# Optimization experiments

Measured on AMD Instinct MI355X. Metric: run time of the kernel, lower is better.

## Reference

```python
import jax, jax.numpy as jnp
import numpy as np

N_NODES = 50000
N_EDGES = 800000
F_IN = 128
HEADS = 4
C_OUT = 32
NEG_SLOPE = 0.2
BN_EPS = 1e-5


def _add_self_loops(edge_index, edge_attr, n):
    # PyG fill_value='mean': self-loop attr = mean of incoming edge attrs per node (0 if none)
    src, dst = edge_index[0], edge_index[1]
    deg = jax.ops.segment_sum(jnp.ones_like(edge_attr[:, 0]), dst, num_segments=n)
    loop_attr = jax.ops.segment_sum(edge_attr, dst, num_segments=n) / jnp.maximum(deg, 1.0)[:, None]
    loop = jnp.arange(n)
    src2 = jnp.concatenate([src, loop])
    dst2 = jnp.concatenate([dst, loop])
    attr2 = jnp.concatenate([edge_attr, loop_attr], axis=0)
    return src2, dst2, attr2


def _segment_softmax(logits, seg, n):
    m = jax.ops.segment_max(logits, seg, num_segments=n)
    m = jnp.where(jnp.isfinite(m), m, 0.0)
    ex = jnp.exp(logits - m[seg])
    s = jax.ops.segment_sum(ex, seg, num_segments=n)
    return ex / s[seg]


def _gatv2(x, src, dst, eattr, Wl, bl, Wr, br, We, att, bias, n):
    # x: [n, F]; returns [n, HEADS*C_OUT]
    xl = (x @ Wl + bl).reshape(n, HEADS, C_OUT)
    xr = (x @ Wr + br).reshape(n, HEADS, C_OUT)
    ea = (eattr @ We).reshape(-1, HEADS, C_OUT)
    xlj = xl[src]                                   # [E, H, C] gather
    msg = jax.nn.leaky_relu(xlj + xr[dst] + ea, NEG_SLOPE)
    logits = jnp.einsum('ehc,hc->eh', msg, att)     # [E, H]
    alpha = _segment_softmax(logits, dst, n)
    out = jax.ops.segment_sum(xlj * alpha[..., None], dst, num_segments=n)
    return out.reshape(n, HEADS * C_OUT) + bias


def _batchnorm(x, gamma, beta):
    mu = x.mean(axis=0)
    var = x.var(axis=0)
    return gamma * (x - mu) * jax.lax.rsqrt(var + BN_EPS) + beta


def setup_inputs() -> dict:
    key = jax.random.key(0)
    ks = jax.random.split(key, 20)
    HC = HEADS * C_OUT
    s = 0.05
    inp = {
        'emb': jax.random.normal(ks[0], (N_NODES, F_IN), dtype=jnp.float32),
        'edge_index': jax.random.randint(ks[1], (2, N_EDGES), 0, N_NODES, dtype=jnp.int64),
        'edge_weight': jax.random.uniform(ks[2], (N_EDGES, 1), dtype=jnp.float32),
        'Wl1': jax.random.normal(ks[3], (F_IN, HC)) * s,
        'bl1': jnp.zeros((HC,), jnp.float32),
        'Wr1': jax.random.normal(ks[4], (F_IN, HC)) * s,
        'br1': jnp.zeros((HC,), jnp.float32),
        'We1': jax.random.normal(ks[5], (1, HC)) * s,
        'att1': jax.random.normal(ks[6], (HEADS, C_OUT)) * s,
        'bias1': jnp.zeros((HC,), jnp.float32),
        'gamma1': jnp.ones((HC,), jnp.float32),
        'beta1': jnp.zeros((HC,), jnp.float32),
        'Wl2': jax.random.normal(ks[7], (HC, HC)) * s,
        'bl2': jnp.zeros((HC,), jnp.float32),
        'Wr2': jax.random.normal(ks[8], (HC, HC)) * s,
        'br2': jnp.zeros((HC,), jnp.float32),
        'We2': jax.random.normal(ks[9], (1, HC)) * s,
        'att2': jax.random.normal(ks[10], (HEADS, C_OUT)) * s,
        'bias2': jnp.zeros((HC,), jnp.float32),
    }
    return inp


def reference(emb, edge_index, edge_weight, Wl1, bl1, Wr1, br1, We1, att1, bias1,
              gamma1, beta1, Wl2, bl2, Wr2, br2, We2, att2, bias2):
    n = emb.shape[0]
    src, dst, eattr = _add_self_loops(edge_index, edge_weight, n)
    h1 = _gatv2(emb, src, dst, eattr, Wl1, bl1, Wr1, br1, We1, att1, bias1, n)
    h1 = jax.nn.elu(_batchnorm(h1, gamma1, beta1))
    h2 = _gatv2(h1, src, dst, eattr, Wl2, bl2, Wr2, br2, We2, att2, bias2, n)
    # fusion: mean over [input_emb, h1, h2] along stacked axis
    return (emb + h1 + h2) / 3.0
```

## Files before the change

kernel.cpp:

```cpp
#include <hip/hip_runtime.h>
#include <hip/hip_bf16.h>
#include <math.h>

#define N_NODES 50000
#define N_EDGES 800000
#define HC 128
#define SLOT 64

#define BM 128
#define NBX ((N_NODES + BM - 1) / BM)
#define NCHK 64
#define EPB (N_EDGES / NCHK)
#define NRNG 4
#define RNG_N (N_NODES / NRNG)
#define RNG_W (RNG_N / 2)
#define NW (N_NODES / 2)
#define NSCAT (NCHK * NRNG)
#define NB2 ((NW + 255) / 256)

typedef short bh8 __attribute__((ext_vector_type(8)));
typedef float f4 __attribute__((ext_vector_type(4)));
typedef float f2 __attribute__((ext_vector_type(2)));

__device__ __forceinline__ unsigned int pk2(float a, float b) {
  return (unsigned int)__bfloat16_as_ushort(__float2bfloat16(a)) |
         ((unsigned int)__bfloat16_as_ushort(__float2bfloat16(b)) << 16);
}
__device__ __forceinline__ float blo(unsigned int u) { return __uint_as_float(u << 16); }
__device__ __forceinline__ float bhi(unsigned int u) { return __uint_as_float(u & 0xffff0000u); }
__device__ __forceinline__ f2 vmax2(f2 a, f2 b) {
#if __has_builtin(__builtin_elementwise_max)
  return __builtin_elementwise_max(a, b);
#else
  f2 r; r.x = fmaxf(a.x, b.x); r.y = fmaxf(a.y, b.y); return r;
#endif
}

__global__ __launch_bounds__(256) void k_histprep(
    const float* __restrict__ Wl1, const float* __restrict__ Wr1,
    const float* __restrict__ Wl2, const float* __restrict__ Wr2,
    unsigned short* __restrict__ WtAll,
    float* __restrict__ chsum, float* __restrict__ chsq,
    const int* __restrict__ ei, unsigned int* __restrict__ counts32) {
  __shared__ unsigned int hist[RNG_W];
  int tid = threadIdx.x, bid = blockIdx.x;
  int gid = bid * 256 + tid;
  {
    int m = gid >> 14;
    int idx = gid & 16383;
    const float* src = (m == 0) ? Wl1 : (m == 1) ? Wr1 : (m == 2) ? Wl2 : Wr2;
    int k = idx >> 7, n = idx & 127;
    WtAll[((size_t)m * HC + n) * HC + k] =
        __bfloat16_as_ushort(__float2bfloat16(src[k * HC + n]));
    if (gid < HC) { chsum[gid] = 0.f; chsq[gid] = 0.f; }
  }
  int c = bid >> 2, r = bid & 3;
  int rb = r * RNG_N;
  for (int w = tid; w < RNG_W; w += 256) hist[w] = 0u;
  __syncthreads();
  const int* dstp = ei + N_EDGES + c * EPB;
  for (int g = tid; g < EPB / 4; g += 256) {
    int4 d4 = *(const int4*)(dstp + g * 4);
    int dl;
    dl = d4.x - rb; if ((unsigned)dl < RNG_N) atomicAdd(&hist[dl >> 1], (dl & 1) ? 0x10000u : 1u);
    dl = d4.y - rb; if ((unsigned)dl < RNG_N) atomicAdd(&hist[dl >> 1], (dl & 1) ? 0x10000u : 1u);
    dl = d4.z - rb; if ((unsigned)dl < RNG_N) atomicAdd(&hist[dl >> 1], (dl & 1) ? 0x10000u : 1u);
    dl = d4.w - rb; if ((unsigned)dl < RNG_N) atomicAdd(&hist[dl >> 1], (dl & 1) ? 0x10000u : 1u);
  }
  __syncthreads();
  unsigned int* dst = counts32 + (size_t)c * NW + r * RNG_W;
  for (int w = tid; w < RNG_W; w += 256) dst[w] = hist[w];
}

__global__ __launch_bounds__(256) void k_scan(const unsigned int* __restrict__ counts32,
                                              unsigned int* __restrict__ bases32,
                                              int* __restrict__ cursor,
                                              int* __restrict__ counts2) {
  __shared__ int dh[80];
  int tid = threadIdx.x;
  int w = blockIdx.x * 256 + tid;
  if (tid < 80) dh[tid] = 0;
  __syncthreads();
  if (w < NW) {
    unsigned int a0 = 0, a1 = 0;
#pragma unroll 4
    for (int b = 0; b < NCHK; ++b) {
      unsigned int v = counts32[(size_t)b * NW + w];
      bases32[(size_t)b * NW + w] = a0 | (a1 << 16);
      a0 += v & 0xffffu;
      a1 += v >> 16;
    }
    cursor[2 * w] = (int)a0;
    cursor[2 * w + 1] = (int)a1;
    atomicAdd(&dh[min((int)a0, SLOT)], 1);
    atomicAdd(&dh[min((int)a1, SLOT)], 1);
  }
  __syncthreads();
  if (tid <= SLOT) counts2[blockIdx.x * 72 + tid] = dh[tid];
}

__global__ __launch_bounds__(256) void k_dprefix(const int* __restrict__ counts2,
                                                 int* __restrict__ bases2) {
  __shared__ int colsum[80], cbase[80];
  int d = threadIdx.x;
  if (d <= SLOT) {
    int s = 0;
    for (int b = 0; b < NB2; ++b) s += counts2[b * 72 + d];
    colsum[d] = s;
  }
  __syncthreads();
  if (d == 0) {
    int a = 0;
    for (int i = 0; i <= SLOT; ++i) { cbase[i] = a; a += colsum[i]; }
  }
  __syncthreads();
  if (d <= SLOT) {
    int a = cbase[d];
    for (int b = 0; b < NB2; ++b) { bases2[b * 72 + d] = a; a += counts2[b * 72 + d]; }
  }
}

__global__ __launch_bounds__(256) void k_scat_g1(
    const int* __restrict__ ei, const float* __restrict__ ew,
    const unsigned int* __restrict__ bases32, unsigned int* __restrict__ slots,
    const float* __restrict__ X, const unsigned short* __restrict__ Wt,
    const float* __restrict__ b0, const float* __restrict__ b1,
    unsigned short* __restrict__ Y0b, float* __restrict__ Y1,
    const int* __restrict__ cursor, const int* __restrict__ bases2,
    int* __restrict__ perm) {
  __shared__ __align__(16) unsigned int lsbuf[16384];
  int tid = threadIdx.x, bid = blockIdx.x;
  if (bid >= NSCAT + NBX) {
    int b2 = bid - NSCAT - NBX;
    int* dcur = (int*)lsbuf;
    if (tid <= SLOT) dcur[tid] = bases2[b2 * 72 + tid];
    __syncthreads();
    for (int i = tid; i < 512; i += 256) {
      int nn = b2 * 512 + i;
      if (nn < N_NODES) {
        int d = min(cursor[nn], SLOT);
        int pos = atomicAdd(&dcur[d], 1);
        perm[pos] = nn;
      }
    }
    return;
  }
  if (bid < NSCAT) {
    int c = bid >> 2, r = bid & 3;
    int rb = r * RNG_N;
    const unsigned int* bp = bases32 + (size_t)c * NW + r * RNG_W;
    for (int w = tid; w < RNG_W; w += 256) lsbuf[w] = bp[w];
    __syncthreads();
    const int* sp = ei + c * EPB;
    const int* dp = ei + N_EDGES + c * EPB;
    const float* wp = ew + c * EPB;
    for (int g = tid; g < EPB / 4; g += 256) {
      int4 s4 = *(const int4*)(sp + g * 4);
      int4 d4 = *(const int4*)(dp + g * 4);
      float4 w4 = *(const float4*)(wp + g * 4);
      int ss[4] = {s4.x, s4.y, s4.z, s4.w};
      int dd[4] = {d4.x, d4.y, d4.z, d4.w};
      float ww[4] = {w4.x, w4.y, w4.z, w4.w};
#pragma unroll
      for (int i = 0; i < 4; ++i) {
        int dl = dd[i] - rb;
        if ((unsigned)dl < RNG_N) {
          unsigned int old = atomicAdd(&lsbuf[dl >> 1], (dl & 1) ? 0x10000u : 1u);
          unsigned int pos = (dl & 1) ? (old >> 16) : (old & 0xffffu);
          unsigned int wq = min((unsigned int)(ww[i] * 65536.f + 0.5f), 65535u);
          if (pos < SLOT)
            slots[(size_t)dd[i] * SLOT + pos] = ((unsigned int)ss[i] << 16) | wq;
        }
      }
    }
    return;
  }
  unsigned short* Xls = (unsigned short*)lsbuf;
  unsigned short* Wls = Xls + 128 * 128;
  int row0 = (bid - NSCAT) * BM;
  {
    int r = tid >> 1;
    int ks = (tid & 1) * 64;
    int gr = row0 + r;
    const float* xp = X + (size_t)gr * HC + ks;
    int sw = r & 15;
#pragma unroll
    for (int i = 0; i < 4; ++i) {
      float f[16];
      if (gr < N_NODES) {
        *(float4*)&f[0] = *(const float4*)(xp + i * 16);
        *(float4*)&f[4] = *(const float4*)(xp + i * 16 + 4);
        *(float4*)&f[8] = *(const float4*)(xp + i * 16 + 8);
        *(float4*)&f[12] = *(const float4*)(xp + i * 16 + 12);
      } else {
#pragma unroll
        for (int j = 0; j < 16; ++j) f[j] = 0.f;
      }
      int kg = (ks >> 3) + i * 2;
      *(uint4*)&Xls[r * 128 + ((kg ^ sw) * 8)] =
          make_uint4(pk2(f[0], f[1]), pk2(f[2], f[3]), pk2(f[4], f[5]), pk2(f[6], f[7]));
      *(uint4*)&Xls[r * 128 + (((kg + 1) ^ sw) * 8)] =
          make_uint4(pk2(f[8], f[9]), pk2(f[10], f[11]), pk2(f[12], f[13]), pk2(f[14], f[15]));
    }
  }
  int lane = tid & 63;
  int wv = tid >> 6;
  int lrow = lane & 15;
  int lq = lane >> 4;
  int rbase = wv * 32;
#pragma unroll
  for (int half = 0; half < 2; ++half) {
    if (half) __syncthreads();
    {
      int n = tid >> 1;
      int ks2 = (tid & 1) * 64;
      const unsigned short* wp = Wt + half * (HC * HC) + n * HC + ks2;
      int swn = n & 15;
#pragma unroll
      for (int g = 0; g < 8; ++g) {
        uint4 v = *(const uint4*)(wp + g * 8);
        int kg = (ks2 >> 3) + g;
        *(uint4*)&Wls[n * 128 + ((kg ^ swn) * 8)] = v;
      }
    }
    __syncthreads();
    f4 acc[2][8];
#pragma unroll
    for (int mt = 0; mt < 2; ++mt)
#pragma unroll
      for (int nt = 0; nt < 8; ++nt) acc[mt][nt] = (f4){0.f, 0.f, 0.f, 0.f};
#pragma unroll
    for (int kk = 0; kk < 4; ++kk) {
      int kg = kk * 4 + lq;
      bh8 a0 = *(const bh8*)&Xls[(rbase + lrow) * 128 + ((kg ^ lrow) * 8)];
      bh8 a1 = *(const bh8*)&Xls[(rbase + 16 + lrow) * 128 + ((kg ^ lrow) * 8)];
#pragma unroll
      for (int nt = 0; nt < 8; ++nt) {
        bh8 b = *(const bh8*)&Wls[(nt * 16 + lrow) * 128 + ((kg ^ lrow) * 8)];
        acc[0][nt] = __builtin_amdgcn_mfma_f32_16x16x32_bf16(a0, b, acc[0][nt], 0, 0, 0);
        acc[1][nt] = __builtin_amdgcn_mfma_f32_16x16x32_bf16(a1, b, acc[1][nt], 0, 0, 0);
      }
    }
    const float* bb = half ? b1 : b0;
    float bv[8];
#pragma unroll
    for (int nt = 0; nt < 8; ++nt) bv[nt] = bb[nt * 16 + lrow];
#pragma unroll
    for (int mt = 0; mt < 2; ++mt) {
#pragma unroll
      for (int rr = 0; rr < 4; ++rr) {
        int gr = row0 + rbase + mt * 16 + lq * 4 + rr;
        if (gr < N_NODES) {
          if (half == 0) {
#pragma unroll
            for (int nt = 0; nt < 8; ++nt)
              Y0b[(size_t)gr * HC + nt * 16 + lrow] =
                  __bfloat16_as_ushort(__float2bfloat16(acc[mt][nt][rr] + bv[nt]));
          } else {
#pragma unroll
            for (int nt = 0; nt < 8; ++nt)
              Y1[(size_t)gr * HC + nt * 16 + lrow] = acc[mt][nt][rr] + bv[nt];
          }
        }
      }
    }
  }
}

__global__ __launch_bounds__(256) void k_gemm2(
    const unsigned short* __restrict__ Xb, const unsigned short* __restrict__ Wt,
    const float* __restrict__ b0, const float* __restrict__ b1,
    unsigned char* __restrict__ Y0f8, float* __restrict__ Y1,
    const float* __restrict__ chsum, const float* __restrict__ chsq,
    const float* __restrict__ gamma, const float* __restrict__ beta) {
  __shared__ __align__(16) unsigned short Xls[128 * 128];
  __shared__ __align__(16) unsigned short Wls[128 * 128];
  __shared__ float ssc[HC], ssh[HC];
  int tid = threadIdx.x;
  if (tid < HC) {
    float mu = chsum[tid] * (1.f / N_NODES);
    float var = chsq[tid] * (1.f / N_NODES) - mu * mu;
    float sc = gamma[tid] * rsqrtf(var + 1e-5f);
    ssc[tid] = sc;
    ssh[tid] = beta[tid] - mu * sc;
  }
  __syncthreads();
  int row0 = blockIdx.x * BM;
  {
    int r = tid >> 1;
    int ks = (tid & 1) * 64;
    int gr = row0 + r;
    const unsigned short* xp = Xb + (size_t)gr * HC + ks;
    int sw = r & 15;
#pragma unroll
    for (int i = 0; i < 4; ++i) {
      float f[16];
      if (gr < N_NODES) {
        uint4 ua = *(const uint4*)(xp + i * 16);
        uint4 ub = *(const uint4*)(xp + i * 16 + 8);
        f[0] = blo(ua.x); f[1] = bhi(ua.x); f[2] = blo(ua.y); f[3] = bhi(ua.y);
        f[4] = blo(ua.z); f[5] = bhi(ua.z); f[6] = blo(ua.w); f[7] = bhi(ua.w);
        f[8] = blo(ub.x); f[9] = bhi(ub.x); f[10] = blo(ub.y); f[11] = bhi(ub.y);
        f[12] = blo(ub.z); f[13] = bhi(ub.z); f[14] = blo(ub.w); f[15] = bhi(ub.w);
      } else {
#pragma unroll
        for (int j = 0; j < 16; ++j) f[j] = 0.f;
      }
#pragma unroll
      for (int j = 0; j < 16; ++j) {
        float y = fmaf(f[j], ssc[ks + i * 16 + j], ssh[ks + i * 16 + j]);
        f[j] = (y > 0.f) ? y : (__expf(y) - 1.f);
      }
      int kg = (ks >> 3) + i * 2;
      *(uint4*)&Xls[r * 128 + ((kg ^ sw) * 8)] =
          make_uint4(pk2(f[0], f[1]), pk2(f[2], f[3]), pk2(f[4], f[5]), pk2(f[6], f[7]));
      *(uint4*)&Xls[r * 128 + (((kg + 1) ^ sw) * 8)] =
          make_uint4(pk2(f[8], f[9]), pk2(f[10], f[11]), pk2(f[12], f[13]), pk2(f[14], f[15]));
    }
  }
  int lane = tid & 63;
  int wv = tid >> 6;
  int lrow = lane & 15;
  int lq = lane >> 4;
  int rbase = wv * 32;
#pragma unroll
  for (int half = 0; half < 2; ++half) {
    if (half) __syncthreads();
    {
      int n = tid >> 1;
      int ks = (tid & 1) * 64;
      const unsigned short* wp = Wt + half * (HC * HC) + n * HC + ks;
      int swn = n & 15;
#pragma unroll
      for (int g = 0; g < 8; ++g) {
        uint4 v = *(const uint4*)(wp + g * 8);
        int kg = (ks >> 3) + g;
        *(uint4*)&Wls[n * 128 + ((kg ^ swn) * 8)] = v;
      }
    }
    __syncthreads();
    f4 acc[2][8];
#pragma unroll
    for (int mt = 0; mt < 2; ++mt)
#pragma unroll
      for (int nt = 0; nt < 8; ++nt) acc[mt][nt] = (f4){0.f, 0.f, 0.f, 0.f};
#pragma unroll
    for (int kk = 0; kk < 4; ++kk) {
      int kg = kk * 4 + lq;
      bh8 a0 = *(const bh8*)&Xls[(rbase + lrow) * 128 + ((kg ^ lrow) * 8)];
      bh8 a1 = *(const bh8*)&Xls[(rbase + 16 + lrow) * 128 + ((kg ^ lrow) * 8)];
#pragma unroll
      for (int nt = 0; nt < 8; ++nt) {
        bh8 b = *(const bh8*)&Wls[(nt * 16 + lrow) * 128 + ((kg ^ lrow) * 8)];
        acc[0][nt] = __builtin_amdgcn_mfma_f32_16x16x32_bf16(a0, b, acc[0][nt], 0, 0, 0);
        acc[1][nt] = __builtin_amdgcn_mfma_f32_16x16x32_bf16(a1, b, acc[1][nt], 0, 0, 0);
      }
    }
    const float* bb = half ? b1 : b0;
    float bv[8];
#pragma unroll
    for (int nt = 0; nt < 8; ++nt) bv[nt] = bb[nt * 16 + lrow];
#pragma unroll
    for (int mt = 0; mt < 2; ++mt) {
#pragma unroll
      for (int rr = 0; rr < 4; ++rr) {
        int gr = row0 + rbase + mt * 16 + lq * 4 + rr;
        if (gr < N_NODES) {
          if (half == 0) {
#pragma unroll
            for (int nt = 0; nt < 8; ++nt) {
              float v = acc[mt][nt][rr] + bv[nt];
              int p = __builtin_amdgcn_cvt_pk_fp8_f32(v, v, 0, false);
              Y0f8[(size_t)gr * HC + nt * 16 + lrow] = (unsigned char)(p & 0xff);
            }
          } else {
#pragma unroll
            for (int nt = 0; nt < 8; ++nt)
              Y1[(size_t)gr * HC + nt * 16 + lrow] = acc[mt][nt][rr] + bv[nt];
          }
        }
      }
    }
  }
}

template <int FINAL, int F8>
__global__ __launch_bounds__(256) void k_gat(
    const void* __restrict__ xlv, const float* __restrict__ xr,
    const int* __restrict__ cursor, const unsigned int* __restrict__ slots,
    const int* __restrict__ perm,
    const float* __restrict__ We, const float* __restrict__ att,
    const float* __restrict__ bias, void* __restrict__ out,
    const float* __restrict__ emb, const unsigned short* __restrict__ h1p,
    const float* __restrict__ chsum, const float* __restrict__ chsq,
    const float* __restrict__ gamma, const float* __restrict__ beta) {
  int g = threadIdx.x >> 5;
  int lane = threadIdx.x & 31;
  int n = perm[blockIdx.x * 8 + g];
  int fi = n * 32 + lane;
  const uint2* xl2 = (const uint2*)xlv;
  const unsigned int* xf = (const unsigned int*)xlv;
  float4 xr4 = ((const float4*)xr)[fi];
  float4 we4 = ((const float4*)We)[lane];
  float4 at4 = ((const float4*)att)[lane];
  const float LOG2E = 1.4426950408889634f;
  const float WSC = 1.f / 65536.f;
  f2 xr01 = {xr4.x, xr4.y}, xr23 = {xr4.z, xr4.w};
  f2 we01 = {we4.x * WSC, we4.y * WSC}, we23 = {we4.z * WSC, we4.w * WSC};
  f2 at01 = {at4.x * LOG2E, at4.y * LOG2E}, at23 = {at4.z * LOG2E, at4.w * LOG2E};
  int deg = min(cursor[n], SLOT);
  int base = n * SLOT;
  int deg32 = min(deg, 32);

  unsigned int ev = (lane < deg32) ? slots[base + lane] : 0u;
  float wsum = (float)(ev & 0xffffu);
#pragma unroll
  for (int m = 16; m >= 1; m >>= 1) wsum += __shfl_xor(wsum, m);

  float l = 0.f;
  f2 o01 = {0.f, 0.f}, o23 = {0.f, 0.f};

  auto decode = [&](uint2 gc, f2& a, f2& b) {
    if (F8) {
      a = __builtin_amdgcn_cvt_pk_f32_fp8((int)gc.x, false);
      b = __builtin_amdgcn_cvt_pk_f32_fp8((int)gc.x, true);
    } else {
      a = (f2){blo(gc.x), bhi(gc.x)};
      b = (f2){blo(gc.y), bhi(gc.y)};
    }
  };
  auto edge_body = [&](float w, uint2 gc, bool valid) {
    f2 a, b;
    decode(gc, a, b);
    f2 m01 = (a + xr01) + w * we01;
    f2 m23 = (b + xr23) + w * we23;
    m01 = vmax2(m01, m01 * 0.2f);
    m23 = vmax2(m23, m23 * 0.2f);
    f2 dp = m01 * at01 + m23 * at23;
    float p = dp.x + dp.y;
    p += __shfl_xor(p, 1);
    p += __shfl_xor(p, 2);
    p += __shfl_xor(p, 4);
#if __has_builtin(__builtin_amdgcn_exp2f)
    float e = valid ? __builtin_amdgcn_exp2f(p) : 0.f;
#else
    float e = valid ? __expf(p * 0.6931471805599453f) : 0.f;
#endif
    l += e;
    o01 = o01 + e * a;
    o23 = o23 + e * b;
  };
  auto fetch = [&](int j, uint2& qq, float& ww) {
    int jc = min(j, deg32 - 1);
    unsigned int evj = __shfl(ev, jc, 32);
    ww = (float)(evj & 0xffffu);
    int s = (int)(evj >> 16);
    if (F8) qq.x = xf[s * 32 + lane];
    else qq = xl2[s * 32 + lane];
  };

  if (deg32 > 0) {
    uint2 q0, q1, q2, q3;
    float w0, w1, w2, w3;
    fetch(0, q0, w0);
    fetch(1, q1, w1);
    fetch(2, q2, w2);
    fetch(3, q3, w3);
    for (int b = 0; b < deg32; b += 4) {
      uint2 c0 = q0, c1 = q1, c2 = q2, c3 = q3;
      float x0 = w0, x1 = w1, x2 = w2, x3 = w3;
      fetch(b + 4, q0, w0);
      fetch(b + 5, q1, w1);
      fetch(b + 6, q2, w2);
      fetch(b + 7, q3, w3);
      edge_body(x0, c0, true);
      edge_body(x1, c1, b + 1 < deg32);
      edge_body(x2, c2, b + 2 < deg32);
      edge_body(x3, c3, b + 3 < deg32);
    }
  }
  if (deg > 32) {
    for (int j = base + 32; j < base + deg; ++j) {
      unsigned int evj = slots[j];
      float w = (float)(evj & 0xffffu);
      wsum += w;
      int s = (int)(evj >> 16);
      uint2 gc;
      if (F8) gc.x = xf[s * 32 + lane];
      else gc = xl2[s * 32 + lane];
      edge_body(w, gc, true);
    }
  }
  {
    float wself = (deg > 0) ? wsum / (float)deg : 0.f;
    uint2 gs;
    if (F8) gs.x = xf[n * 32 + lane];
    else gs = xl2[n * 32 + lane];
    edge_body(wself, gs, true);
  }

  float inv = 1.f / l;
  float4 o = make_float4(o01.x, o01.y, o23.x, o23.y);
  float4 b4 = ((const float4*)bias)[lane];
  float4 r;
  r.x = fmaf(o.x, inv, b4.x);
  r.y = fmaf(o.y, inv, b4.y);
  r.z = fmaf(o.z, inv, b4.z);
  r.w = fmaf(o.w, inv, b4.w);
  if (FINAL) {
    float4 e4 = ((const float4*)emb)[fi];
    uint2 hh = ((const uint2*)h1p)[fi];
    float4 h4;
    h4.x = blo(hh.x); h4.y = bhi(hh.x); h4.z = blo(hh.y); h4.w = bhi(hh.y);
    float4 cs = ((const float4*)chsum)[lane];
    float4 cq = ((const float4*)chsq)[lane];
    float4 gm = ((const float4*)gamma)[lane];
    float4 bt = ((const float4*)beta)[lane];
    const float invN = 1.f / N_NODES;
    float4 sc4, sh4;
    {
      float mu = cs.x * invN, var = cq.x * invN - mu * mu;
      sc4.x = gm.x * rsqrtf(var + 1e-5f); sh4.x = bt.x - mu * sc4.x;
      mu = cs.y * invN; var = cq.y * invN - mu * mu;
      sc4.y = gm.y * rsqrtf(var + 1e-5f); sh4.y = bt.y - mu * sc4.y;
      mu = cs.z * invN; var = cq.z * invN - mu * mu;
      sc4.z = gm.z * rsqrtf(var + 1e-5f); sh4.z = bt.z - mu * sc4.z;
      mu = cs.w * invN; var = cq.w * invN - mu * mu;
      sc4.w = gm.w * rsqrtf(var + 1e-5f); sh4.w = bt.w - mu * sc4.w;
    }
    float4 h;
    h.x = fmaf(h4.x, sc4.x, sh4.x);
    h.y = fmaf(h4.y, sc4.y, sh4.y);
    h.z = fmaf(h4.z, sc4.z, sh4.z);
    h.w = fmaf(h4.w, sc4.w, sh4.w);
    h.x = (h.x > 0.f) ? h.x : (__expf(h.x) - 1.f);
    h.y = (h.y > 0.f) ? h.y : (__expf(h.y) - 1.f);
    h.z = (h.z > 0.f) ? h.z : (__expf(h.z) - 1.f);
    h.w = (h.w > 0.f) ? h.w : (__expf(h.w) - 1.f);
    const float k3 = 1.f / 3.f;
    r.x = (e4.x + h.x + r.x) * k3;
    r.y = (e4.y + h.y + r.y) * k3;
    r.z = (e4.z + h.z + r.z) * k3;
    r.w = (e4.w + h.w + r.w) * k3;
    ((float4*)out)[fi] = r;
  } else {
    ((uint2*)out)[fi] = make_uint2(pk2(r.x, r.y), pk2(r.z, r.w));
  }
}

#define BN_ROWS 200
__global__ __launch_bounds__(256) void k_bnstats(const unsigned short* __restrict__ h1b,
                                                 float* __restrict__ chsum,
                                                 float* __restrict__ chsq) {
  int c2 = threadIdx.x & 63;
  int g = threadIdx.x >> 6;
  int r0 = blockIdx.x * BN_ROWS;
  float s0 = 0.f, s1 = 0.f, q0 = 0.f, q1 = 0.f;
  const unsigned int* h32 = (const unsigned int*)h1b;
  for (int r = r0 + g; r < r0 + BN_ROWS; r += 4) {
    unsigned int u = h32[(size_t)r * 64 + c2];
    float a = blo(u), b = bhi(u);
    s0 += a; q0 += a * a;
    s1 += b; q1 += b * b;
  }
  __shared__ float sh[256][4];
  sh[threadIdx.x][0] = s0; sh[threadIdx.x][1] = q0;
  sh[threadIdx.x][2] = s1; sh[threadIdx.x][3] = q1;
  __syncthreads();
  if (g == 0) {
    float ts0 = 0.f, tq0 = 0.f, ts1 = 0.f, tq1 = 0.f;
#pragma unroll
    for (int gg = 0; gg < 4; ++gg) {
      ts0 += sh[gg * 64 + c2][0]; tq0 += sh[gg * 64 + c2][1];
      ts1 += sh[gg * 64 + c2][2]; tq1 += sh[gg * 64 + c2][3];
    }
    atomicAdd(chsum + 2 * c2, ts0);
    atomicAdd(chsq + 2 * c2, tq0);
    atomicAdd(chsum + 2 * c2 + 1, ts1);
    atomicAdd(chsq + 2 * c2 + 1, tq1);
  }
}

extern "C" void kernel_launch(void* const* d_in, const int* in_sizes, int n_in,
                              void* d_out, int out_size, void* d_ws, size_t ws_size,
                              hipStream_t stream) {
  const float* emb = (const float*)d_in[0];
  const int* ei = (const int*)d_in[1];
  const float* ew = (const float*)d_in[2];
  const float* Wl1 = (const float*)d_in[3];
  const float* bl1 = (const float*)d_in[4];
  const float* Wr1 = (const float*)d_in[5];
  const float* br1 = (const float*)d_in[6];
  const float* We1 = (const float*)d_in[7];
  const float* att1 = (const float*)d_in[8];
  const float* bias1 = (const float*)d_in[9];
  const float* gamma1 = (const float*)d_in[10];
  const float* beta1 = (const float*)d_in[11];
  const float* Wl2 = (const float*)d_in[12];
  const float* bl2 = (const float*)d_in[13];
  const float* Wr2 = (const float*)d_in[14];
  const float* br2 = (const float*)d_in[15];
  const float* We2 = (const float*)d_in[16];
  const float* att2 = (const float*)d_in[17];
  const float* bias2 = (const float*)d_in[18];
  float* out = (float*)d_out;

  char* wsb = (char*)d_ws;
  size_t off = 0;
  auto alloc = [&](size_t bytes) -> void* {
    void* p = (void*)(wsb + off);
    off += (bytes + 255) & ~(size_t)255;
    return p;
  };
  int* cursor = (int*)alloc((size_t)N_NODES * 4);
  float* chsum = (float*)alloc(HC * 4);
  float* chsq = (float*)alloc(HC * 4);
  unsigned short* WtAll = (unsigned short*)alloc((size_t)4 * HC * HC * 2);
  unsigned int* counts32 = (unsigned int*)alloc((size_t)NCHK * NW * 4);
  unsigned int* bases32 = (unsigned int*)alloc((size_t)NCHK * NW * 4);
  unsigned int* slots = (unsigned int*)alloc((size_t)N_NODES * SLOT * 4);
  unsigned short* xlb = (unsigned short*)alloc((size_t)N_NODES * HC * 2);
  unsigned char* xlf8 = (unsigned char*)alloc((size_t)N_NODES * HC);
  float* xr = (float*)alloc((size_t)N_NODES * HC * 4);
  unsigned short* h1b = (unsigned short*)alloc((size_t)N_NODES * HC * 2);
  int* counts2 = (int*)alloc((size_t)NB2 * 72 * 4);
  int* bases2 = (int*)alloc((size_t)NB2 * 72 * 4);
  int* perm = (int*)alloc((size_t)N_NODES * 4);

  k_histprep<<<NSCAT, 256, 0, stream>>>(Wl1, Wr1, Wl2, Wr2, WtAll, chsum, chsq,
                                        ei, counts32);
  k_scan<<<NB2, 256, 0, stream>>>(counts32, bases32, cursor, counts2);
  k_dprefix<<<1, 256, 0, stream>>>(counts2, bases2);
  k_scat_g1<<<NSCAT + NBX + NB2, 256, 0, stream>>>(ei, ew, bases32, slots, emb,
                                                   WtAll, bl1, br1, xlb, xr,
                                                   cursor, bases2, perm);
  k_gat<0, 0><<<N_NODES / 8, 256, 0, stream>>>(xlb, xr, cursor, slots, perm, We1,
                                               att1, bias1, (void*)h1b, nullptr,
                                               nullptr, nullptr, nullptr, nullptr,
                                               nullptr);
  k_bnstats<<<N_NODES / BN_ROWS, 256, 0, stream>>>(h1b, chsum, chsq);
  k_gemm2<<<NBX, 256, 0, stream>>>(h1b, WtAll + 2 * HC * HC, bl2, br2, xlf8, xr,
                                   chsum, chsq, gamma1, beta1);
  k_gat<1, 1><<<N_NODES / 8, 256, 0, stream>>>(xlf8, xr, cursor, slots, perm, We2,
                                               att2, bias2, (void*)out, emb, h1b,
                                               chsum, chsq, gamma1, beta1);
}
```

Baseline: 278.3 us.

## Use 16 lanes per node with 8 channels each; fuse dprefix into scan

The GAT aggregation kernel now gives each node 16 lanes, each handling 8 channels, instead of 32 lanes with 4 channels. This lets it use wider 16-byte gathers, needs fewer shuffle steps, and packs 16 nodes per block, while the software prefetch depth drops from 4 edges to 2. Separately, the single-block degree prefix kernel is folded into k_scan through a last-block-done atomic ticket, removing one launch. The trade-offs are more registers per thread and less memory-level parallelism per lane.

```diff
diff --git a/kernel.cpp b/kernel.cpp
--- a/kernel.cpp
+++ b/kernel.cpp
@@ -41,7 +41,8 @@
     const float* __restrict__ Wl2, const float* __restrict__ Wr2,
     unsigned short* __restrict__ WtAll,
     float* __restrict__ chsum, float* __restrict__ chsq,
-    const int* __restrict__ ei, unsigned int* __restrict__ counts32) {
+    const int* __restrict__ ei, unsigned int* __restrict__ counts32,
+    int* __restrict__ done) {
   __shared__ unsigned int hist[RNG_W];
   int tid = threadIdx.x, bid = blockIdx.x;
   int gid = bid * 256 + tid;
@@ -53,6 +54,7 @@
     WtAll[((size_t)m * HC + n) * HC + k] =
         __bfloat16_as_ushort(__float2bfloat16(src[k * HC + n]));
     if (gid < HC) { chsum[gid] = 0.f; chsq[gid] = 0.f; }
+    if (gid == 256) *done = 0;
   }
   int c = bid >> 2, r = bid & 3;
   int rb = r * RNG_N;
@@ -75,7 +77,9 @@
 __global__ __launch_bounds__(256) void k_scan(const unsigned int* __restrict__ counts32,
                                               unsigned int* __restrict__ bases32,
                                               int* __restrict__ cursor,
-                                              int* __restrict__ counts2) {
+                                              int* __restrict__ counts2,
+                                              int* __restrict__ bases2,
+                                              int* __restrict__ done) {
   __shared__ int dh[80];
   int tid = threadIdx.x;
   int w = blockIdx.x * 256 + tid;
@@ -97,26 +101,28 @@
   }
   __syncthreads();
   if (tid <= SLOT) counts2[blockIdx.x * 72 + tid] = dh[tid];
-}
-
-__global__ __launch_bounds__(256) void k_dprefix(const int* __restrict__ counts2,
-                                                 int* __restrict__ bases2) {
-  __shared__ int colsum[80], cbase[80];
-  int d = threadIdx.x;
-  if (d <= SLOT) {
-    int s = 0;
-    for (int b = 0; b < NB2; ++b) s += counts2[b * 72 + d];
-    colsum[d] = s;
-  }
+  __threadfence();
+  __shared__ int ticket;
+  if (tid == 0) ticket = atomicAdd(done, 1);
   __syncthreads();
-  if (d == 0) {
-    int a = 0;
-    for (int i = 0; i <= SLOT; ++i) { cbase[i] = a; a += colsum[i]; }
-  }
-  __syncthreads();
-  if (d <= SLOT) {
-    int a = cbase[d];
-    for (int b = 0; b < NB2; ++b) { bases2[b * 72 + d] = a; a += counts2[b * 72 + d]; }
+  if (ticket == NB2 - 1) {
+    __threadfence();
+    __shared__ int colsum[80], cbase[80];
+    if (tid <= SLOT) {
+      int s = 0;
+      for (int b = 0; b < NB2; ++b) s += counts2[b * 72 + tid];
+      colsum[tid] = s;
+    }
+    __syncthreads();
+    if (tid == 0) {
+      int a = 0;
+      for (int i = 0; i <= SLOT; ++i) { cbase[i] = a; a += colsum[i]; }
+    }
+    __syncthreads();
+    if (tid <= SLOT) {
+      int a = cbase[tid];
+      for (int b = 0; b < NB2; ++b) { bases2[b * 72 + tid] = a; a += counts2[b * 72 + tid]; }
+    }
   }
 }
 
@@ -394,89 +400,93 @@
     const float* __restrict__ emb, const unsigned short* __restrict__ h1p,
     const float* __restrict__ chsum, const float* __restrict__ chsq,
     const float* __restrict__ gamma, const float* __restrict__ beta) {
-  int g = threadIdx.x >> 5;
-  int lane = threadIdx.x & 31;
-  int n = perm[blockIdx.x * 8 + g];
-  int fi = n * 32 + lane;
-  const uint2* xl2 = (const uint2*)xlv;
-  const unsigned int* xf = (const unsigned int*)xlv;
-  float4 xr4 = ((const float4*)xr)[fi];
-  float4 we4 = ((const float4*)We)[lane];
-  float4 at4 = ((const float4*)att)[lane];
+  int g = threadIdx.x >> 4;
+  int lane = threadIdx.x & 15;
+  int n = perm[blockIdx.x * 16 + g];
+  int ci = lane * 2;
+  int fr = n * 32 + ci;
+  const uint4* xl4 = (const uint4*)xlv;
+  const uint2* xf2 = (const uint2*)xlv;
+  float4 xa = ((const float4*)xr)[fr], xb = ((const float4*)xr)[fr + 1];
+  float4 wa = ((const float4*)We)[ci], wb = ((const float4*)We)[ci + 1];
+  float4 aa = ((const float4*)att)[ci], ab = ((const float4*)att)[ci + 1];
   const float LOG2E = 1.4426950408889634f;
   const float WSC = 1.f / 65536.f;
-  f2 xr01 = {xr4.x, xr4.y}, xr23 = {xr4.z, xr4.w};
-  f2 we01 = {we4.x * WSC, we4.y * WSC}, we23 = {we4.z * WSC, we4.w * WSC};
-  f2 at01 = {at4.x * LOG2E, at4.y * LOG2E}, at23 = {at4.z * LOG2E, at4.w * LOG2E};
+  f2 xr01 = {xa.x, xa.y}, xr23 = {xa.z, xa.w}, xr45 = {xb.x, xb.y}, xr67 = {xb.z, xb.w};
+  f2 we01 = {wa.x * WSC, wa.y * WSC}, we23 = {wa.z * WSC, wa.w * WSC};
+  f2 we45 = {wb.x * WSC, wb.y * WSC}, we67 = {wb.z * WSC, wb.w * WSC};
+  f2 at01 = {aa.x * LOG2E, aa.y * LOG2E}, at23 = {aa.z * LOG2E, aa.w * LOG2E};
+  f2 at45 = {ab.x * LOG2E, ab.y * LOG2E}, at67 = {ab.z * LOG2E, ab.w * LOG2E};
   int deg = min(cursor[n], SLOT);
   int base = n * SLOT;
   int deg32 = min(deg, 32);
 
-  unsigned int ev = (lane < deg32) ? slots[base + lane] : 0u;
-  float wsum = (float)(ev & 0xffffu);
-#pragma unroll
-  for (int m = 16; m >= 1; m >>= 1) wsum += __shfl_xor(wsum, m);
+  unsigned int ev0 = (lane < deg32) ? slots[base + lane] : 0u;
+  unsigned int ev1 = (16 + lane < deg32) ? slots[base + 16 + lane] : 0u;
+  float wsum = (float)(ev0 & 0xffffu) + (float)(ev1 & 0xffffu);
+#pragma unroll
+  for (int m = 8; m >= 1; m >>= 1) wsum += __shfl_xor(wsum, m);
 
   float l = 0.f;
-  f2 o01 = {0.f, 0.f}, o23 = {0.f, 0.f};
-
-  auto decode = [&](uint2 gc, f2& a, f2& b) {
+  f2 o01 = {0.f, 0.f}, o23 = {0.f, 0.f}, o45 = {0.f, 0.f}, o67 = {0.f, 0.f};
+
+  auto edge_body = [&](float w, uint4 q, bool valid) {
+    f2 a0, a1, a2, a3;
     if (F8) {
-      a = __builtin_amdgcn_cvt_pk_f32_fp8((int)gc.x, false);
-      b = __builtin_amdgcn_cvt_pk_f32_fp8((int)gc.x, true);
+      a0 = __builtin_amdgcn_cvt_pk_f32_fp8((int)q.x, false);
+      a1 = __builtin_amdgcn_cvt_pk_f32_fp8((int)q.x, true);
+      a2 = __builtin_amdgcn_cvt_pk_f32_fp8((int)q.y, false);
+      a3 = __builtin_amdgcn_cvt_pk_f32_fp8((int)q.y, true);
     } else {
-      a = (f2){blo(gc.x), bhi(gc.x)};
-      b = (f2){blo(gc.y), bhi(gc.y)};
-    }
-  };
-  auto edge_body = [&](float w, uint2 gc, bool valid) {
-    f2 a, b;
-    decode(gc, a, b);
-    f2 m01 = (a + xr01) + w * we01;
-    f2 m23 = (b + xr23) + w * we23;
-    m01 = vmax2(m01, m01 * 0.2f);
-    m23 = vmax2(m23, m23 * 0.2f);
-    f2 dp = m01 * at01 + m23 * at23;
-    float p = dp.x + dp.y;
+      a0 = (f2){blo(q.x), bhi(q.x)};
+      a1 = (f2){blo(q.y), bhi(q.y)};
+      a2 = (f2){blo(q.z), bhi(q.z)};
+      a3 = (f2){blo(q.w), bhi(q.w)};
+    }
+    f2 m0 = (a0 + xr01) + w * we01;
+    f2 m1 = (a1 + xr23) + w * we23;
+    f2 m2 = (a2 + xr45) + w * we45;
+    f2 m3 = (a3 + xr67) + w * we67;
+    m0 = vmax2(m0, m0 * 0.2f);
+    m1 = vmax2(m1, m1 * 0.2f);
+    m2 = vmax2(m2, m2 * 0.2f);
+    m3 = vmax2(m3, m3 * 0.2f);
+    f2 t = m0 * at01 + m1 * at23;
+    t = t + (m2 * at45 + m3 * at67);
+    float p = t.x + t.y;
     p += __shfl_xor(p, 1);
     p += __shfl_xor(p, 2);
-    p += __shfl_xor(p, 4);
 #if __has_builtin(__builtin_amdgcn_exp2f)
     float e = valid ? __builtin_amdgcn_exp2f(p) : 0.f;
 #else
     float e = valid ? __expf(p * 0.6931471805599453f) : 0.f;
 #endif
     l += e;
-    o01 = o01 + e * a;
-    o23 = o23 + e * b;
+    o01 = o01 + e * a0;
+    o23 = o23 + e * a1;
+    o45 = o45 + e * a2;
+    o67 = o67 + e * a3;
   };
-  auto fetch = [&](int j, uint2& qq, float& ww) {
+  auto fetch = [&](int j, uint4& q, float& w) {
     int jc = min(j, deg32 - 1);
-    unsigned int evj = __shfl(ev, jc, 32);
-    ww = (float)(evj & 0xffffu);
+    unsigned int evs = (jc & 16) ? ev1 : ev0;
+    unsigned int evj = __shfl(evs, jc & 15, 16);
+    w = (float)(evj & 0xffffu);
     int s = (int)(evj >> 16);
-    if (F8) qq.x = xf[s * 32 + lane];
-    else qq = xl2[s * 32 + lane];
+    if (F8) { uint2 t = xf2[s * 16 + lane]; q.x = t.x; q.y = t.y; }
+    else q = xl4[s * 16 + lane];
   };
 
   if (deg32 > 0) {
-    uint2 q0, q1, q2, q3;
-    float w0, w1, w2, w3;
+    uint4 q0, q1;
+    float w0, w1;
     fetch(0, q0, w0);
     fetch(1, q1, w1);
-    fetch(2, q2, w2);
-    fetch(3, q3, w3);
-    for (int b = 0; b < deg32; b += 4) {
-      uint2 c0 = q0, c1 = q1, c2 = q2, c3 = q3;
-      float x0 = w0, x1 = w1, x2 = w2, x3 = w3;
-      fetch(b + 4, q0, w0);
-      fetch(b + 5, q1, w1);
-      fetch(b + 6, q2, w2);
-      fetch(b + 7, q3, w3);
-      edge_body(x0, c0, true);
-      edge_body(x1, c1, b + 1 < deg32);
-      edge_body(x2, c2, b + 2 < deg32);
-      edge_body(x3, c3, b + 3 < deg32);
+    for (int b = 0; b < deg32; b += 2) {
+      edge_body(w0, q0, true);
+      fetch(b + 2, q0, w0);
+      edge_body(w1, q1, b + 1 < deg32);
+      fetch(b + 3, q1, w1);
     }
   }
   if (deg > 32) {
@@ -485,66 +495,58 @@
       float w = (float)(evj & 0xffffu);
       wsum += w;
       int s = (int)(evj >> 16);
-      uint2 gc;
-      if (F8) gc.x = xf[s * 32 + lane];
-      else gc = xl2[s * 32 + lane];
+      uint4 gc;
+      if (F8) { uint2 t = xf2[s * 16 + lane]; gc.x = t.x; gc.y = t.y; }
+      else gc = xl4[s * 16 + lane];
       edge_body(w, gc, true);
     }
   }
   {
     float wself = (deg > 0) ? wsum / (float)deg : 0.f;
-    uint2 gs;
-    if (F8) gs.x = xf[n * 32 + lane];
-    else gs = xl2[n * 32 + lane];
+    uint4 gs;
+    if (F8) { uint2 t = xf2[n * 16 + lane]; gs.x = t.x; gs.y = t.y; }
+    else gs = xl4[n * 16 + lane];
     edge_body(wself, gs, true);
   }
 
   float inv = 1.f / l;
-  float4 o = make_float4(o01.x, o01.y, o23.x, o23.y);
-  float4 b4 = ((const float4*)bias)[lane];
-  float4 r;
-  r.x = fmaf(o.x, inv, b4.x);
-  r.y = fmaf(o.y, inv, b4.y);
-  r.z = fmaf(o.z, inv, b4.z);
-  r.w = fmaf(o.w, inv, b4.w);
+  float4 ba = ((const float4*)bias)[ci], bbv = ((const float4*)bias)[ci + 1];
+  float r0 = fmaf(o01.x, inv, ba.x), r1 = fmaf(o01.y, inv, ba.y);
+  float r2 = fmaf(o23.x, inv, ba.z), r3 = fmaf(o23.y, inv, ba.w);
+  float r4 = fmaf(o45.x, inv, bbv.x), r5 = fmaf(o45.y, inv, bbv.y);
+  float r6 = fmaf(o67.x, inv, bbv.z), r7 = fmaf(o67.y, inv, bbv.w);
   if (FINAL) {
-    float4 e4 = ((const float4*)emb)[fi];
-    uint2 hh = ((const uint2*)h1p)[fi];
-    float4 h4;
-    h4.x = blo(hh.x); h4.y = bhi(hh.x); h4.z = blo(hh.y); h4.w = bhi(hh.y);
-    float4 cs = ((const float4*)chsum)[lane];
-    float4 cq = ((const float4*)chsq)[lane];
-    float4 gm = ((const float4*)gamma)[lane];
-    float4 bt = ((const float4*)beta)[lane];
+    float4 ea = ((const float4*)emb)[fr], eb = ((const float4*)emb)[fr + 1];
+    uint4 hh = ((const uint4*)h1p)[n * 16 + lane];
+    float hv[8] = {blo(hh.x), bhi(hh.x), blo(hh.y), bhi(hh.y),
+                   blo(hh.z), bhi(hh.z), blo(hh.w), bhi(hh.w)};
+    float4 csa = ((const float4*)chsum)[ci], csb = ((const float4*)chsum)[ci + 1];
+    float4 cqa = ((const float4*)chsq)[ci], cqb = ((const float4*)chsq)[ci + 1];
+    float4 gma = ((const float4*)gamma)[ci], gmb = ((const float4*)gamma)[ci + 1];
+    float4 bta = ((const float4*)beta)[ci], btb = ((const float4*)beta)[ci + 1];
+    float cs[8] = {csa.x, csa.y, csa.z, csa.w, csb.x, csb.y, csb.z, csb.w};
+    float cq[8] = {cqa.x, cqa.y, cqa.z, cqa.w, cqb.x, cqb.y, cqb.z, cqb.w};
+    float gm[8] = {gma.x, gma.y, gma.z, gma.w, gmb.x, gmb.y, gmb.z, gmb.w};
+    float bt[8] = {bta.x, bta.y, bta.z, bta.w, btb.x, btb.y, btb.z, btb.w};
+    float ev4[8] = {ea.x, ea.y, ea.z, ea.w, eb.x, eb.y, eb.z, eb.w};
+    float rr[8] = {r0, r1, r2, r3, r4, r5, r6, r7};
     const float invN = 1.f / N_NODES;
-    float4 sc4, sh4;
-    {
-      float mu = cs.x * invN, var = cq.x * invN - mu * mu;
-      sc4.x = gm.x * rsqrtf(var + 1e-5f); sh4.x = bt.x - mu * sc4.x;
-      mu = cs.y * invN; var = cq.y * invN - mu * mu;
-      sc4.y = gm.y * rsqrtf(var + 1e-5f); sh4.y = bt.y - mu * sc4.y;
-      mu = cs.z * invN; var = cq.z * invN - mu * mu;
-      sc4.z = gm.z * rsqrtf(var + 1e-5f); sh4.z = bt.z - mu * sc4.z;
-      mu = cs.w * invN; var = cq.w * invN - mu * mu;
-      sc4.w = gm.w * rsqrtf(var + 1e-5f); sh4.w = bt.w - mu * sc4.w;
-    }
-    float4 h;
-    h.x = fmaf(h4.x, sc4.x, sh4.x);
-    h.y = fmaf(h4.y, sc4.y, sh4.y);
-    h.z = fmaf(h4.z, sc4.z, sh4.z);
-    h.w = fmaf(h4.w, sc4.w, sh4.w);
-    h.x = (h.x > 0.f) ? h.x : (__expf(h.x) - 1.f);
-    h.y = (h.y > 0.f) ? h.y : (__expf(h.y) - 1.f);
-    h.z = (h.z > 0.f) ? h.z : (__expf(h.z) - 1.f);
-    h.w = (h.w > 0.f) ? h.w : (__expf(h.w) - 1.f);
     const float k3 = 1.f / 3.f;
-    r.x = (e4.x + h.x + r.x) * k3;
-    r.y = (e4.y + h.y + r.y) * k3;
-    r.z = (e4.z + h.z + r.z) * k3;
-    r.w = (e4.w + h.w + r.w) * k3;
-    ((float4*)out)[fi] = r;
+#pragma unroll
+    for (int k = 0; k < 8; ++k) {
+      float mu = cs[k] * invN;
+      float var = cq[k] * invN - mu * mu;
+      float sc = gm[k] * rsqrtf(var + 1e-5f);
+      float sh = bt[k] - mu * sc;
+      float h = fmaf(hv[k], sc, sh);
+      h = (h > 0.f) ? h : (__expf(h) - 1.f);
+      rr[k] = (ev4[k] + h + rr[k]) * k3;
+    }
+    ((float4*)out)[fr] = make_float4(rr[0], rr[1], rr[2], rr[3]);
+    ((float4*)out)[fr + 1] = make_float4(rr[4], rr[5], rr[6], rr[7]);
   } else {
-    ((uint2*)out)[fi] = make_uint2(pk2(r.x, r.y), pk2(r.z, r.w));
+    ((uint4*)out)[n * 16 + lane] =
+        make_uint4(pk2(r0, r1), pk2(r2, r3), pk2(r4, r5), pk2(r6, r7));
   }
 }
 
@@ -626,22 +628,22 @@
   int* counts2 = (int*)alloc((size_t)NB2 * 72 * 4);
   int* bases2 = (int*)alloc((size_t)NB2 * 72 * 4);
   int* perm = (int*)alloc((size_t)N_NODES * 4);
+  int* done = (int*)alloc(256);
 
   k_histprep<<<NSCAT, 256, 0, stream>>>(Wl1, Wr1, Wl2, Wr2, WtAll, chsum, chsq,
-                                        ei, counts32);
-  k_scan<<<NB2, 256, 0, stream>>>(counts32, bases32, cursor, counts2);
-  k_dprefix<<<1, 256, 0, stream>>>(counts2, bases2);
+                                        ei, counts32, done);
+  k_scan<<<NB2, 256, 0, stream>>>(counts32, bases32, cursor, counts2, bases2, done);
   k_scat_g1<<<NSCAT + NBX + NB2, 256, 0, stream>>>(ei, ew, bases32, slots, emb,
                                                    WtAll, bl1, br1, xlb, xr,
                                                    cursor, bases2, perm);
-  k_gat<0, 0><<<N_NODES / 8, 256, 0, stream>>>(xlb, xr, cursor, slots, perm, We1,
-                                               att1, bias1, (void*)h1b, nullptr,
-                                               nullptr, nullptr, nullptr, nullptr,
-                                               nullptr);
+  k_gat<0, 0><<<N_NODES / 16, 256, 0, stream>>>(xlb, xr, cursor, slots, perm, We1,
+                                                att1, bias1, (void*)h1b, nullptr,
+                                                nullptr, nullptr, nullptr, nullptr,
+                                                nullptr);
   k_bnstats<<<N_NODES / BN_ROWS, 256, 0, stream>>>(h1b, chsum, chsq);
   k_gemm2<<<NBX, 256, 0, stream>>>(h1b, WtAll + 2 * HC * HC, bl2, br2, xlf8, xr,
                                    chsum, chsq, gamma1, beta1);
-  k_gat<1, 1><<<N_NODES / 8, 256, 0, stream>>>(xlf8, xr, cursor, slots, perm, We2,
-                                               att2, bias2, (void*)out, emb, h1b,
-                                               chsum, chsq, gamma1, beta1);
-}
+  k_gat<1, 1><<<N_NODES / 16, 256, 0, stream>>>(xlf8, xr, cursor, slots, perm, We2,
+                                                att2, bias2, (void*)out, emb, h1b,
+                                                chsum, chsq, gamma1, beta1);
+}
```

New measurement: 281.9 us. About the same (+1.3%).
